# Kernel tuning notes

Measured on AMD Instinct MI355X. Metric: run time of the kernel, lower is better.

Reference implementation:

```python
import jax, jax.numpy as jnp
import numpy as np

N_NODES = 10000
N_EDGES = 640000
N_GRAPHS = 64
IN_FEATS = 128
H_FEATS = 128


def setup_inputs() -> dict:
    key = jax.random.key(0)
    ks = jax.random.split(key, 8)
    in_feat = jax.random.normal(ks[0], (N_NODES, IN_FEATS), dtype=jnp.float32)
    src = jax.random.randint(ks[1], (N_EDGES,), 0, N_NODES, dtype=jnp.int32)
    dst = jax.random.randint(ks[2], (N_EDGES,), 0, N_NODES, dtype=jnp.int32)
    graph_ids = jnp.sort(jax.random.randint(ks[3], (N_NODES,), 0, N_GRAPHS, dtype=jnp.int32))
    s1 = 1.0 / np.sqrt(IN_FEATS)
    s2 = 1.0 / np.sqrt(H_FEATS)
    W1 = jax.random.uniform(ks[4], (IN_FEATS, H_FEATS), jnp.float32, -s1, s1)
    b1 = jnp.zeros((H_FEATS,), jnp.float32)
    W2 = jax.random.uniform(ks[5], (H_FEATS, H_FEATS), jnp.float32, -s2, s2)
    b2 = jnp.zeros((H_FEATS,), jnp.float32)
    Wd = jax.random.uniform(ks[6], (H_FEATS, 1), jnp.float32, -s2, s2)
    bd = jnp.zeros((1,), jnp.float32)
    return {"in_feat": in_feat, "src": src, "dst": dst, "graph_ids": graph_ids,
            "W1": W1, "b1": b1, "W2": W2, "b2": b2, "Wd": Wd, "bd": bd}


def _graph_conv(x, src, dst, norm_src, norm_dst, W, b):
    # DGL GraphConv, norm='both': D_dst^{-1/2} A D_src^{-1/2} X W + b
    x = x * norm_src[:, None]
    agg = jax.ops.segment_sum(x[src], dst, num_segments=N_NODES)  # scatter-add over edges
    agg = agg * norm_dst[:, None]
    return agg @ W + b


def reference(in_feat, src, dst, graph_ids, W1, b1, W2, b2, Wd, bd):
    ones_e = jnp.ones((N_EDGES,), in_feat.dtype)
    out_deg = jax.ops.segment_sum(ones_e, src, num_segments=N_NODES)
    in_deg = jax.ops.segment_sum(ones_e, dst, num_segments=N_NODES)
    norm_src = jnp.where(out_deg > 0, out_deg, 1.0) ** -0.5
    norm_dst = jnp.where(in_deg > 0, in_deg, 1.0) ** -0.5

    h = jax.nn.relu(_graph_conv(in_feat, src, dst, norm_src, norm_dst, W1, b1))
    h = jax.nn.relu(_graph_conv(h, src, dst, norm_src, norm_dst, W2, b2))

    # dgl.mean_nodes: per-graph mean of node features
    counts = jax.ops.segment_sum(jnp.ones((N_NODES,), h.dtype), graph_ids, num_segments=N_GRAPHS)
    pooled = jax.ops.segment_sum(h, graph_ids, num_segments=N_GRAPHS)
    pooled = pooled / jnp.maximum(counts, 1.0)[:, None]

    out = pooled @ Wd + bd  # [G, 1]
    return out.squeeze(-1)
```

## Files before the change

kernel.cpp:

```cpp
#include <hip/hip_runtime.h>

#define N_NODES 10000
#define N_EDGES 640000
#define N_GRAPHS 64
#define FEATS 128

#define NSLICE 128
#define EPS (N_EDGES / NSLICE)
#define CAP 160

static inline size_t align_up(size_t x, size_t a) { return (x + a - 1) & ~(a - 1); }

__global__ __launch_bounds__(256) void hist_kernel(const int* __restrict__ src,
                                                   const int* __restrict__ dst,
                                                   int* __restrict__ counts,
                                                   int* __restrict__ scounts) {
    __shared__ int h[N_NODES];
    const int tid = threadIdx.x;
    const int b = blockIdx.x;
    const bool is_dst = (b < NSLICE);
    const int slice = is_dst ? b : b - NSLICE;
    const int* col = is_dst ? dst : src;
    int* outp = (is_dst ? counts : scounts) + slice * N_NODES;

    for (int i = tid; i < N_NODES; i += 256) h[i] = 0;
    __syncthreads();
    const int4* c4 = (const int4*)(col + slice * EPS);
    for (int i = tid; i < EPS / 4; i += 256) {
        int4 v = c4[i];
        atomicAdd(&h[v.x], 1);
        atomicAdd(&h[v.y], 1);
        atomicAdd(&h[v.z], 1);
        atomicAdd(&h[v.w], 1);
    }
    __syncthreads();
    for (int i = tid; i < N_NODES; i += 256) outp[i] = h[i];
}

__global__ __launch_bounds__(256) void degnorm_base_kernel(int* __restrict__ counts,
                                                           const int* __restrict__ scounts,
                                                           const int* __restrict__ gids,
                                                           int* __restrict__ deg_in,
                                                           float* __restrict__ norm_src,
                                                           float* __restrict__ norm_dst,
                                                           int* __restrict__ graph_cnt) {
    __shared__ int gcnt[N_GRAPHS];
    const int tid = threadIdx.x;
    if (tid < N_GRAPHS) gcnt[tid] = 0;
    __syncthreads();
    int n = blockIdx.x * 256 + tid;
    if (n < N_NODES) {
        int run = n * CAP;
        for (int s = 0; s < NSLICE; s++) {
            int c = counts[s * N_NODES + n];
            counts[s * N_NODES + n] = run;
            run += c;
        }
        int di = run - n * CAP;
        int dou = 0;
        for (int s = 0; s < NSLICE; s++) dou += scounts[s * N_NODES + n];
        deg_in[n] = di;
        norm_dst[n] = rsqrtf((float)(di < 1 ? 1 : di));
        norm_src[n] = rsqrtf((float)(dou < 1 ? 1 : dou));
        atomicAdd(&gcnt[gids[n]], 1);
    }
    __syncthreads();
    if (tid < N_GRAPHS && gcnt[tid]) atomicAdd(&graph_cnt[tid], gcnt[tid]);
}

__global__ __launch_bounds__(256) void scatter_kernel(const int* __restrict__ src,
                                                      const int* __restrict__ dst,
                                                      const int* __restrict__ base,
                                                      const float* __restrict__ norm_src,
                                                      int* __restrict__ sorted_src,
                                                      float* __restrict__ sorted_ns) {
    __shared__ int cur[N_NODES];
    const int tid = threadIdx.x;
    const int s = blockIdx.x;
    for (int i = tid; i < N_NODES; i += 256) cur[i] = base[s * N_NODES + i];
    __syncthreads();
    const int4* s4 = (const int4*)(src + s * EPS);
    const int4* d4 = (const int4*)(dst + s * EPS);
    for (int i = tid; i < EPS / 4; i += 256) {
        int4 sv = s4[i];
        int4 dv = d4[i];
        int p;
        p = atomicAdd(&cur[dv.x], 1); sorted_src[p] = sv.x; sorted_ns[p] = norm_src[sv.x];
        p = atomicAdd(&cur[dv.y], 1); sorted_src[p] = sv.y; sorted_ns[p] = norm_src[sv.y];
        p = atomicAdd(&cur[dv.z], 1); sorted_src[p] = sv.z; sorted_ns[p] = norm_src[sv.z];
        p = atomicAdd(&cur[dv.w], 1); sorted_src[p] = sv.w; sorted_ns[p] = norm_src[sv.w];
    }
}

__global__ __launch_bounds__(256) void aggregate_kernel(const float* __restrict__ X,
                                                        const int* __restrict__ sorted_src,
                                                        const float* __restrict__ sorted_ns,
                                                        const int* __restrict__ deg_in,
                                                        const float* __restrict__ norm_dst,
                                                        float* __restrict__ out) {
    const int tid = threadIdx.x;
    const int wave = tid >> 6, lane = tid & 63;
    const int half = lane >> 5, l32 = lane & 31;
    const int n = blockIdx.x * 4 + wave;
    const int start = n * CAP;
    const int cnt = deg_in[n];
    const float4* __restrict__ x4 = (const float4*)X;
    float4 acc = make_float4(0.f, 0.f, 0.f, 0.f);

    int c = half;
    for (; c + 6 < cnt; c += 8) {
        const int e0 = start + c, e1 = e0 + 2, e2 = e0 + 4, e3 = e0 + 6;
        const int   i0 = sorted_src[e0]; const float s0 = sorted_ns[e0];
        const int   i1 = sorted_src[e1]; const float s1 = sorted_ns[e1];
        const int   i2 = sorted_src[e2]; const float s2 = sorted_ns[e2];
        const int   i3 = sorted_src[e3]; const float s3 = sorted_ns[e3];
        float4 v0 = x4[i0 * 32 + l32];
        float4 v1 = x4[i1 * 32 + l32];
        float4 v2 = x4[i2 * 32 + l32];
        float4 v3 = x4[i3 * 32 + l32];
        acc.x = fmaf(s0, v0.x, acc.x); acc.y = fmaf(s0, v0.y, acc.y);
        acc.z = fmaf(s0, v0.z, acc.z); acc.w = fmaf(s0, v0.w, acc.w);
        acc.x = fmaf(s1, v1.x, acc.x); acc.y = fmaf(s1, v1.y, acc.y);
        acc.z = fmaf(s1, v1.z, acc.z); acc.w = fmaf(s1, v1.w, acc.w);
        acc.x = fmaf(s2, v2.x, acc.x); acc.y = fmaf(s2, v2.y, acc.y);
        acc.z = fmaf(s2, v2.z, acc.z); acc.w = fmaf(s2, v2.w, acc.w);
        acc.x = fmaf(s3, v3.x, acc.x); acc.y = fmaf(s3, v3.y, acc.y);
        acc.z = fmaf(s3, v3.z, acc.z); acc.w = fmaf(s3, v3.w, acc.w);
    }
    for (; c < cnt; c += 2) {
        const int e = start + c;
        const int i = sorted_src[e];
        const float s = sorted_ns[e];
        float4 v = x4[i * 32 + l32];
        acc.x = fmaf(s, v.x, acc.x); acc.y = fmaf(s, v.y, acc.y);
        acc.z = fmaf(s, v.z, acc.z); acc.w = fmaf(s, v.w, acc.w);
    }
    acc.x += __shfl_xor(acc.x, 32); acc.y += __shfl_xor(acc.y, 32);
    acc.z += __shfl_xor(acc.z, 32); acc.w += __shfl_xor(acc.w, 32);
    if (half == 0) {
        const float nd = norm_dst[n];
        float4 o = make_float4(acc.x * nd, acc.y * nd, acc.z * nd, acc.w * nd);
        ((float4*)out)[n * 32 + l32] = o;
    }
}

__global__ __launch_bounds__(256) void gemm_relu_kernel(const float* __restrict__ A,
                                                        const float* __restrict__ W,
                                                        const float* __restrict__ bias,
                                                        float* __restrict__ out) {
    __shared__ float As[16 * FEATS];
    int tid = threadIdx.x;
    int nb = blockIdx.x * 16;
    const float4* av = (const float4*)(A + (size_t)nb * FEATS);
    float4* sv = (float4*)As;
    sv[tid]       = av[tid];
    sv[tid + 256] = av[tid + 256];
    __syncthreads();
    int fg = (tid & 31) << 2;
    int r  = tid >> 5;
    const float* a0p = As + r * FEATS;
    const float* a1p = As + (r + 8) * FEATS;
    float4 acc0 = make_float4(0.f, 0.f, 0.f, 0.f);
    float4 acc1 = make_float4(0.f, 0.f, 0.f, 0.f);
#pragma unroll 4
    for (int k = 0; k < FEATS; k++) {
        float a0 = a0p[k];
        float a1 = a1p[k];
        float4 w = *(const float4*)(W + k * FEATS + fg);
        acc0.x = fmaf(a0, w.x, acc0.x); acc0.y = fmaf(a0, w.y, acc0.y);
        acc0.z = fmaf(a0, w.z, acc0.z); acc0.w = fmaf(a0, w.w, acc0.w);
        acc1.x = fmaf(a1, w.x, acc1.x); acc1.y = fmaf(a1, w.y, acc1.y);
        acc1.z = fmaf(a1, w.z, acc1.z); acc1.w = fmaf(a1, w.w, acc1.w);
    }
    float4 bb = *(const float4*)(bias + fg);
    int gn0 = nb + r, gn1 = nb + r + 8;
    float4 o0, o1;
    o0.x = fmaxf(acc0.x + bb.x, 0.f); o0.y = fmaxf(acc0.y + bb.y, 0.f);
    o0.z = fmaxf(acc0.z + bb.z, 0.f); o0.w = fmaxf(acc0.w + bb.w, 0.f);
    o1.x = fmaxf(acc1.x + bb.x, 0.f); o1.y = fmaxf(acc1.y + bb.y, 0.f);
    o1.z = fmaxf(acc1.z + bb.z, 0.f); o1.w = fmaxf(acc1.w + bb.w, 0.f);
    *(float4*)(out + (size_t)gn0 * FEATS + fg) = o0;
    *(float4*)(out + (size_t)gn1 * FEATS + fg) = o1;
}

__global__ __launch_bounds__(256) void gemm_relu_pool_kernel(const float* __restrict__ A,
                                                             const float* __restrict__ W,
                                                             const float* __restrict__ bias,
                                                             const float* __restrict__ Wd,
                                                             const int* __restrict__ gids,
                                                             float* __restrict__ graph_sum) {
    __shared__ float As[16 * FEATS];
    __shared__ float bins[N_GRAPHS];
    int tid = threadIdx.x;
    int nb = blockIdx.x * 16;
    const float4* av = (const float4*)(A + (size_t)nb * FEATS);
    float4* sv = (float4*)As;
    sv[tid]       = av[tid];
    sv[tid + 256] = av[tid + 256];
    if (tid < N_GRAPHS) bins[tid] = 0.f;
    __syncthreads();
    int fg = (tid & 31) << 2;
    int r  = tid >> 5;
    const float* a0p = As + r * FEATS;
    const float* a1p = As + (r + 8) * FEATS;
    float4 acc0 = make_float4(0.f, 0.f, 0.f, 0.f);
    float4 acc1 = make_float4(0.f, 0.f, 0.f, 0.f);
#pragma unroll 4
    for (int k = 0; k < FEATS; k++) {
        float a0 = a0p[k];
        float a1 = a1p[k];
        float4 w = *(const float4*)(W + k * FEATS + fg);
        acc0.x = fmaf(a0, w.x, acc0.x); acc0.y = fmaf(a0, w.y, acc0.y);
        acc0.z = fmaf(a0, w.z, acc0.z); acc0.w = fmaf(a0, w.w, acc0.w);
        acc1.x = fmaf(a1, w.x, acc1.x); acc1.y = fmaf(a1, w.y, acc1.y);
        acc1.z = fmaf(a1, w.z, acc1.z); acc1.w = fmaf(a1, w.w, acc1.w);
    }
    float4 bb = *(const float4*)(bias + fg);
    float4 wd = *(const float4*)(Wd + fg);
    float p0 = fmaxf(acc0.x + bb.x, 0.f) * wd.x + fmaxf(acc0.y + bb.y, 0.f) * wd.y +
               fmaxf(acc0.z + bb.z, 0.f) * wd.z + fmaxf(acc0.w + bb.w, 0.f) * wd.w;
    float p1 = fmaxf(acc1.x + bb.x, 0.f) * wd.x + fmaxf(acc1.y + bb.y, 0.f) * wd.y +
               fmaxf(acc1.z + bb.z, 0.f) * wd.z + fmaxf(acc1.w + bb.w, 0.f) * wd.w;
#pragma unroll
    for (int d = 16; d >= 1; d >>= 1) {
        p0 += __shfl_down(p0, d);
        p1 += __shfl_down(p1, d);
    }
    if ((tid & 31) == 0) {
        int gn0 = nb + r, gn1 = nb + r + 8;
        atomicAdd(&bins[gids[gn0]], p0);
        atomicAdd(&bins[gids[gn1]], p1);
    }
    __syncthreads();
    if (tid < N_GRAPHS) {
        float v = bins[tid];
        if (v != 0.f) atomicAdd(&graph_sum[tid], v);
    }
}

__global__ __launch_bounds__(64) void final_kernel(const float* __restrict__ graph_sum,
                                                   const int* __restrict__ graph_cnt,
                                                   const float* __restrict__ bd,
                                                   float* __restrict__ out) {
    int g = threadIdx.x;
    if (g < N_GRAPHS) {
        out[g] = graph_sum[g] / fmaxf((float)graph_cnt[g], 1.f) + bd[0];
    }
}

extern "C" void kernel_launch(void* const* d_in, const int* in_sizes, int n_in,
                              void* d_out, int out_size, void* d_ws, size_t ws_size,
                              hipStream_t stream) {
    const float* in_feat = (const float*)d_in[0];
    const int*   src     = (const int*)d_in[1];
    const int*   dst     = (const int*)d_in[2];
    const int*   gids    = (const int*)d_in[3];
    const float* W1      = (const float*)d_in[4];
    const float* b1      = (const float*)d_in[5];
    const float* W2      = (const float*)d_in[6];
    const float* b2      = (const float*)d_in[7];
    const float* Wd      = (const float*)d_in[8];
    const float* bd      = (const float*)d_in[9];
    float* out = (float*)d_out;

    char* ws = (char*)d_ws;
    size_t off = 0;
    int* graph_cnt = (int*)(ws + off); off += N_GRAPHS * 4;
    float* graph_sum = (float*)(ws + off); off += N_GRAPHS * 4;
    size_t zero_bytes = off;
    off = align_up(off, 512);
    int* counts  = (int*)(ws + off); off += (size_t)NSLICE * N_NODES * 4;
    off = align_up(off, 512);
    int* scounts = (int*)(ws + off); off += (size_t)NSLICE * N_NODES * 4;
    off = align_up(off, 512);
    int* deg_in  = (int*)(ws + off); off += N_NODES * 4;
    off = align_up(off, 512);
    float* norm_src = (float*)(ws + off); off += N_NODES * 4;
    off = align_up(off, 512);
    float* norm_dst = (float*)(ws + off); off += N_NODES * 4;
    off = align_up(off, 512);
    int* sorted_src = (int*)(ws + off); off += (size_t)N_NODES * CAP * 4 + 4096;
    off = align_up(off, 512);
    float* sorted_ns = (float*)(ws + off); off += (size_t)N_NODES * CAP * 4 + 4096;
    off = align_up(off, 512);
    float* agg1 = (float*)(ws + off); off += (size_t)N_NODES * FEATS * 4;
    off = align_up(off, 512);
    float* h    = (float*)(ws + off); off += (size_t)N_NODES * FEATS * 4;
    off = align_up(off, 512);
    float* agg2 = (float*)(ws + off); off += (size_t)N_NODES * FEATS * 4;
    (void)ws_size;

    hipMemsetAsync(ws, 0, zero_bytes, stream);

    hist_kernel<<<2 * NSLICE, 256, 0, stream>>>(src, dst, counts, scounts);
    degnorm_base_kernel<<<(N_NODES + 255) / 256, 256, 0, stream>>>(counts, scounts, gids,
                                                                   deg_in, norm_src, norm_dst,
                                                                   graph_cnt);
    scatter_kernel<<<NSLICE, 256, 0, stream>>>(src, dst, counts, norm_src,
                                               sorted_src, sorted_ns);

    aggregate_kernel<<<N_NODES / 4, 256, 0, stream>>>(in_feat, sorted_src, sorted_ns,
                                                      deg_in, norm_dst, agg1);
    gemm_relu_kernel<<<N_NODES / 16, 256, 0, stream>>>(agg1, W1, b1, h);

    aggregate_kernel<<<N_NODES / 4, 256, 0, stream>>>(h, sorted_src, sorted_ns,
                                                      deg_in, norm_dst, agg2);
    gemm_relu_pool_kernel<<<N_NODES / 16, 256, 0, stream>>>(agg2, W2, b2, Wd, gids,
                                                            graph_sum);

    final_kernel<<<1, 64, 0, stream>>>(graph_sum, graph_cnt, bd, out);
}
```

Before: 194.3 us.

## Prescale node features by source norm instead of storing per-edge norms

Moves the D_src^{-1/2} scaling from a per-edge weight array onto the node features. Layer 1 gets its scaling from a new prescale kernel, and layer 2 gets it folded into the first GEMM epilogue. This drops the sorted_ns array, its gather in the scatter kernel, and the per-edge loads and FMAs in aggregation, leaving plain adds. The aggregate loop is unrolled to 8 outstanding gathers, and the slice count is halved to cut histogram and prefix work. The cost is one extra elementwise pass over the input features and less parallelism in the hist and scatter stages.

```diff
diff --git a/kernel.cpp b/kernel.cpp
--- a/kernel.cpp
+++ b/kernel.cpp
@@ -5,7 +5,7 @@
 #define N_GRAPHS 64
 #define FEATS 128
 
-#define NSLICE 128
+#define NSLICE 64
 #define EPS (N_EDGES / NSLICE)
 #define CAP 160
 
@@ -71,9 +71,7 @@
 __global__ __launch_bounds__(256) void scatter_kernel(const int* __restrict__ src,
                                                       const int* __restrict__ dst,
                                                       const int* __restrict__ base,
-                                                      const float* __restrict__ norm_src,
-                                                      int* __restrict__ sorted_src,
-                                                      float* __restrict__ sorted_ns) {
+                                                      int* __restrict__ sorted_src) {
     __shared__ int cur[N_NODES];
     const int tid = threadIdx.x;
     const int s = blockIdx.x;
@@ -85,16 +83,28 @@
         int4 sv = s4[i];
         int4 dv = d4[i];
         int p;
-        p = atomicAdd(&cur[dv.x], 1); sorted_src[p] = sv.x; sorted_ns[p] = norm_src[sv.x];
-        p = atomicAdd(&cur[dv.y], 1); sorted_src[p] = sv.y; sorted_ns[p] = norm_src[sv.y];
-        p = atomicAdd(&cur[dv.z], 1); sorted_src[p] = sv.z; sorted_ns[p] = norm_src[sv.z];
-        p = atomicAdd(&cur[dv.w], 1); sorted_src[p] = sv.w; sorted_ns[p] = norm_src[sv.w];
+        p = atomicAdd(&cur[dv.x], 1); sorted_src[p] = sv.x;
+        p = atomicAdd(&cur[dv.y], 1); sorted_src[p] = sv.y;
+        p = atomicAdd(&cur[dv.z], 1); sorted_src[p] = sv.z;
+        p = atomicAdd(&cur[dv.w], 1); sorted_src[p] = sv.w;
+    }
+}
+
+__global__ __launch_bounds__(256) void prescale_kernel(const float* __restrict__ in_feat,
+                                                       const float* __restrict__ norm_src,
+                                                       float* __restrict__ xs) {
+    int i = blockIdx.x * 256 + threadIdx.x;
+    if (i < N_NODES * (FEATS / 4)) {
+        int n = i >> 5;
+        float4 v = ((const float4*)in_feat)[i];
+        float s = norm_src[n];
+        v.x *= s; v.y *= s; v.z *= s; v.w *= s;
+        ((float4*)xs)[i] = v;
     }
 }
 
 __global__ __launch_bounds__(256) void aggregate_kernel(const float* __restrict__ X,
                                                         const int* __restrict__ sorted_src,
-                                                        const float* __restrict__ sorted_ns,
                                                         const int* __restrict__ deg_in,
                                                         const float* __restrict__ norm_dst,
                                                         float* __restrict__ out) {
@@ -108,32 +118,22 @@
     float4 acc = make_float4(0.f, 0.f, 0.f, 0.f);
 
     int c = half;
-    for (; c + 6 < cnt; c += 8) {
-        const int e0 = start + c, e1 = e0 + 2, e2 = e0 + 4, e3 = e0 + 6;
-        const int   i0 = sorted_src[e0]; const float s0 = sorted_ns[e0];
-        const int   i1 = sorted_src[e1]; const float s1 = sorted_ns[e1];
-        const int   i2 = sorted_src[e2]; const float s2 = sorted_ns[e2];
-        const int   i3 = sorted_src[e3]; const float s3 = sorted_ns[e3];
-        float4 v0 = x4[i0 * 32 + l32];
-        float4 v1 = x4[i1 * 32 + l32];
-        float4 v2 = x4[i2 * 32 + l32];
-        float4 v3 = x4[i3 * 32 + l32];
-        acc.x = fmaf(s0, v0.x, acc.x); acc.y = fmaf(s0, v0.y, acc.y);
-        acc.z = fmaf(s0, v0.z, acc.z); acc.w = fmaf(s0, v0.w, acc.w);
-        acc.x = fmaf(s1, v1.x, acc.x); acc.y = fmaf(s1, v1.y, acc.y);
-        acc.z = fmaf(s1, v1.z, acc.z); acc.w = fmaf(s1, v1.w, acc.w);
-        acc.x = fmaf(s2, v2.x, acc.x); acc.y = fmaf(s2, v2.y, acc.y);
-        acc.z = fmaf(s2, v2.z, acc.z); acc.w = fmaf(s2, v2.w, acc.w);
-        acc.x = fmaf(s3, v3.x, acc.x); acc.y = fmaf(s3, v3.y, acc.y);
-        acc.z = fmaf(s3, v3.z, acc.z); acc.w = fmaf(s3, v3.w, acc.w);
+    for (; c + 14 < cnt; c += 16) {
+        int idx[8];
+#pragma unroll
+        for (int k = 0; k < 8; k++) idx[k] = sorted_src[start + c + 2 * k];
+        float4 v[8];
+#pragma unroll
+        for (int k = 0; k < 8; k++) v[k] = x4[idx[k] * 32 + l32];
+#pragma unroll
+        for (int k = 0; k < 8; k++) {
+            acc.x += v[k].x; acc.y += v[k].y; acc.z += v[k].z; acc.w += v[k].w;
+        }
     }
     for (; c < cnt; c += 2) {
-        const int e = start + c;
-        const int i = sorted_src[e];
-        const float s = sorted_ns[e];
+        int i = sorted_src[start + c];
         float4 v = x4[i * 32 + l32];
-        acc.x = fmaf(s, v.x, acc.x); acc.y = fmaf(s, v.y, acc.y);
-        acc.z = fmaf(s, v.z, acc.z); acc.w = fmaf(s, v.w, acc.w);
+        acc.x += v.x; acc.y += v.y; acc.z += v.z; acc.w += v.w;
     }
     acc.x += __shfl_xor(acc.x, 32); acc.y += __shfl_xor(acc.y, 32);
     acc.z += __shfl_xor(acc.z, 32); acc.w += __shfl_xor(acc.w, 32);
@@ -144,10 +144,11 @@
     }
 }
 
-__global__ __launch_bounds__(256) void gemm_relu_kernel(const float* __restrict__ A,
-                                                        const float* __restrict__ W,
-                                                        const float* __restrict__ bias,
-                                                        float* __restrict__ out) {
+__global__ __launch_bounds__(256) void gemm_relu_scale_kernel(const float* __restrict__ A,
+                                                              const float* __restrict__ W,
+                                                              const float* __restrict__ bias,
+                                                              const float* __restrict__ scale,
+                                                              float* __restrict__ out) {
     __shared__ float As[16 * FEATS];
     int tid = threadIdx.x;
     int nb = blockIdx.x * 16;
@@ -174,11 +175,12 @@
     }
     float4 bb = *(const float4*)(bias + fg);
     int gn0 = nb + r, gn1 = nb + r + 8;
+    float s0 = scale[gn0], s1 = scale[gn1];
     float4 o0, o1;
-    o0.x = fmaxf(acc0.x + bb.x, 0.f); o0.y = fmaxf(acc0.y + bb.y, 0.f);
-    o0.z = fmaxf(acc0.z + bb.z, 0.f); o0.w = fmaxf(acc0.w + bb.w, 0.f);
-    o1.x = fmaxf(acc1.x + bb.x, 0.f); o1.y = fmaxf(acc1.y + bb.y, 0.f);
-    o1.z = fmaxf(acc1.z + bb.z, 0.f); o1.w = fmaxf(acc1.w + bb.w, 0.f);
+    o0.x = fmaxf(acc0.x + bb.x, 0.f) * s0; o0.y = fmaxf(acc0.y + bb.y, 0.f) * s0;
+    o0.z = fmaxf(acc0.z + bb.z, 0.f) * s0; o0.w = fmaxf(acc0.w + bb.w, 0.f) * s0;
+    o1.x = fmaxf(acc1.x + bb.x, 0.f) * s1; o1.y = fmaxf(acc1.y + bb.y, 0.f) * s1;
+    o1.z = fmaxf(acc1.z + bb.z, 0.f) * s1; o1.w = fmaxf(acc1.w + bb.w, 0.f) * s1;
     *(float4*)(out + (size_t)gn0 * FEATS + fg) = o0;
     *(float4*)(out + (size_t)gn1 * FEATS + fg) = o1;
 }
@@ -281,7 +283,7 @@
     off = align_up(off, 512);
     int* sorted_src = (int*)(ws + off); off += (size_t)N_NODES * CAP * 4 + 4096;
     off = align_up(off, 512);
-    float* sorted_ns = (float*)(ws + off); off += (size_t)N_NODES * CAP * 4 + 4096;
+    float* xs   = (float*)(ws + off); off += (size_t)N_NODES * FEATS * 4;
     off = align_up(off, 512);
     float* agg1 = (float*)(ws + off); off += (size_t)N_NODES * FEATS * 4;
     off = align_up(off, 512);
@@ -296,15 +298,14 @@
     degnorm_base_kernel<<<(N_NODES + 255) / 256, 256, 0, stream>>>(counts, scounts, gids,
                                                                    deg_in, norm_src, norm_dst,
                                                                    graph_cnt);
-    scatter_kernel<<<NSLICE, 256, 0, stream>>>(src, dst, counts, norm_src,
-                                               sorted_src, sorted_ns);
-
-    aggregate_kernel<<<N_NODES / 4, 256, 0, stream>>>(in_feat, sorted_src, sorted_ns,
-                                                      deg_in, norm_dst, agg1);
-    gemm_relu_kernel<<<N_NODES / 16, 256, 0, stream>>>(agg1, W1, b1, h);
-
-    aggregate_kernel<<<N_NODES / 4, 256, 0, stream>>>(h, sorted_src, sorted_ns,
-                                                      deg_in, norm_dst, agg2);
+    scatter_kernel<<<NSLICE, 256, 0, stream>>>(src, dst, counts, sorted_src);
+    prescale_kernel<<<(N_NODES * (FEATS / 4) + 255) / 256, 256, 0, stream>>>(in_feat,
+                                                                             norm_src, xs);
+
+    aggregate_kernel<<<N_NODES / 4, 256, 0, stream>>>(xs, sorted_src, deg_in, norm_dst, agg1);
+    gemm_relu_scale_kernel<<<N_NODES / 16, 256, 0, stream>>>(agg1, W1, b1, norm_src, h);
+
+    aggregate_kernel<<<N_NODES / 4, 256, 0, stream>>>(h, sorted_src, deg_in, norm_dst, agg2);
     gemm_relu_pool_kernel<<<N_NODES / 16, 256, 0, stream>>>(agg2, W2, b2, Wd, gids,
                                                             graph_sum);
 
```

New measurement: 194.0 us. About the same (-0.2%).
